# Kernel tuning notes

Measured on AMD Instinct MI355X. Metric: run time of the kernel, lower is better.

Reference implementation:

```python
import jax, jax.numpy as jnp
import numpy as np

HEADS = 16
D_H = 64
ALPHA = 1.0


def _skew(QEr):
    # Music-Transformer skew: (b,h,n,n) -> relative-to-absolute
    b, h, i, j = QEr.shape
    pad = jnp.pad(QEr, ((0, 0), (0, 0), (0, 0), (1, 0)))  # (b,h,i,j+1)
    return pad.reshape(b, h, j + 1, i)[:, :, 1:, :]  # (b,h,i,j)


def _gather_bias(q, table, idx, heads):
    # q: (b,h,i,d); table: (S,d); idx: (b,i,j) int -> (b,h,i,j)
    b, h, i, d = q.shape
    QE = jnp.einsum('bhid,sd->bhis', q, table)  # (b,h,i,S)
    idx_b = jnp.broadcast_to(idx[:, None, :, :], (b, h, i, idx.shape[-1]))
    return jnp.take_along_axis(QE, idx_b, axis=-1)


def setup_inputs() -> dict:
    key = jax.random.key(0)
    ks = jax.random.split(key, 16)
    b, n, dim = 2, 1024, 1024
    d_h = dim // HEADS
    inp = {
        'x': jax.random.normal(ks[0], (b, n, dim), dtype=jnp.float32),
        'rel_bar': jax.random.randint(ks[1], (b, n, n), 0, 17, dtype=jnp.int32),
        'rel_position': jax.random.randint(ks[2], (b, n, n), 0, 96, dtype=jnp.int32),
        'rel_octave': jax.random.randint(ks[3], (b, n, n), 0, 25, dtype=jnp.int32),
        'rel_semitone': jax.random.randint(ks[4], (b, n, n), 0, 13, dtype=jnp.int32),
        'Wq': jax.random.normal(ks[5], (dim, dim), dtype=jnp.float32) * 0.02,
        'Wk': jax.random.normal(ks[6], (dim, dim), dtype=jnp.float32) * 0.02,
        'Wv': jax.random.normal(ks[7], (dim, dim), dtype=jnp.float32) * 0.02,
        'Wo': jax.random.normal(ks[8], (dim, dim), dtype=jnp.float32) * 0.02,
        'Er': jax.random.normal(ks[9], (n, d_h), dtype=jnp.float32),
        'Er_bar': jax.random.normal(ks[10], (16, d_h), dtype=jnp.float32),
        'Er_position': jax.random.normal(ks[11], (95, d_h), dtype=jnp.float32),
        'Er_octave': jax.random.normal(ks[12], (24, d_h), dtype=jnp.float32),
        'Er_semitone': jax.random.normal(ks[13], (12, d_h), dtype=jnp.float32),
    }
    return inp


def reference(x, rel_bar, rel_position, rel_octave, rel_semitone,
              Wq, Wk, Wv, Wo, Er, Er_bar, Er_position, Er_octave, Er_semitone):
    b, n, dim = x.shape
    h, d = HEADS, dim // HEADS

    def split_heads(t):
        return t.reshape(b, n, h, d).transpose(0, 2, 1, 3)  # (b,h,n,d)

    q = split_heads(x @ Wq.T)
    k = split_heads(x @ Wk.T)
    v = split_heads(x @ Wv.T)

    QK_t = jnp.einsum('bhid,bhjd->bhij', q, k)

    # relative-index bias (Music-Transformer style)
    QEr = jnp.einsum('bhid,jd->bhij', q, Er)  # start = max_seq_len - n = 0
    Srel = _skew(QEr)

    zrow = jnp.zeros((1, d), dtype=x.dtype)
    S_bar = _gather_bias(q, jnp.concatenate([Er_bar, zrow]), rel_bar, h)
    S_position = _gather_bias(q, jnp.concatenate([Er_position, zrow]), rel_position, h)
    S_octave = _gather_bias(q, jnp.concatenate([Er_octave, zrow]), rel_octave, h)
    S_semitone = _gather_bias(q, jnp.concatenate([Er_semitone, zrow]), rel_semitone, h)

    S_time = S_bar + S_position
    S_pitch = S_octave + S_semitone

    scores = (QK_t + Srel + ALPHA * (S_time + S_pitch)) / jnp.sqrt(jnp.asarray(d, x.dtype))
    causal = jnp.tril(jnp.ones((n, n), dtype=bool))
    scores = jnp.where(causal[None, None], scores, jnp.asarray(-1e9, x.dtype))
    attn = jax.nn.softmax(scores, axis=-1)

    out = jnp.einsum('bhij,bhjd->bhid', attn, v)
    out = out.transpose(0, 2, 1, 3).reshape(b, n, dim)
    return out @ Wo.T
```

## Files before the change

kernel.cpp:

```cpp
#include <hip/hip_runtime.h>


using bf16x8 = __attribute__((ext_vector_type(8))) short;
using f32x4  = __attribute__((ext_vector_type(4))) float;

__device__ __forceinline__ float bf2f(unsigned short u) {
  unsigned x = ((unsigned)u) << 16;
  float f;
  __builtin_memcpy(&f, &x, 4);
  return f;
}
__device__ __forceinline__ unsigned short f2bf(float f) {
  unsigned x;
  __builtin_memcpy(&x, &f, 4);
  unsigned r = (x + 0x7FFFu + ((x >> 16) & 1u)) >> 16;
  return (unsigned short)r;
}

union B8 { bf16x8 v; unsigned short u[8]; };

__global__ __launch_bounds__(256) void prep(
    const float* __restrict__ x,  const float* __restrict__ Wq,
    const float* __restrict__ Wk, const float* __restrict__ Wv,
    const float* __restrict__ Wo, const float* __restrict__ Er,
    const int* __restrict__ rb, const int* __restrict__ rp,
    const int* __restrict__ ro, const int* __restrict__ rs,
    const float* __restrict__ Tb, const float* __restrict__ Tp,
    const float* __restrict__ To, const float* __restrict__ Ts,
    unsigned short* __restrict__ x_bf, unsigned short* __restrict__ Wqkv,
    unsigned short* __restrict__ Wo_bf, unsigned short* __restrict__ Er_bf,
    unsigned* __restrict__ Pidx, unsigned short* __restrict__ Tpad)
{
  const int bid = blockIdx.x;
  const int tid = threadIdx.x;
  if (bid < 1024) {
    const int total = 1589248;
    for (int i = bid * 256 + tid; i < total; i += 1024 * 256) {
      const float4* s4;
      ushort4* d4;
      if (i < 524288)       { s4 = (const float4*)x  + i;           d4 = (ushort4*)x_bf  + i; }
      else if (i < 786432)  { s4 = (const float4*)Wq + (i-524288);  d4 = (ushort4*)Wqkv  + (i-524288); }
      else if (i < 1048576) { s4 = (const float4*)Wk + (i-786432);  d4 = (ushort4*)Wqkv  + (i-786432) + 262144; }
      else if (i < 1310720) { s4 = (const float4*)Wv + (i-1048576); d4 = (ushort4*)Wqkv  + (i-1048576) + 524288; }
      else if (i < 1572864) { s4 = (const float4*)Wo + (i-1310720); d4 = (ushort4*)Wo_bf + (i-1310720); }
      else                  { s4 = (const float4*)Er + (i-1572864); d4 = (ushort4*)Er_bf + (i-1572864); }
      const float4 v = *s4;
      ushort4 o;
      o.x = f2bf(v.x); o.y = f2bf(v.y); o.z = f2bf(v.z); o.w = f2bf(v.w);
      *d4 = o;
    }
  } else if (bid < 2048) {
    for (int i = (bid - 1024) * 256 + tid; i < 524288; i += 1024 * 256) {
      const int4 a = ((const int4*)rb)[i];
      const int4 b = ((const int4*)rp)[i];
      const int4 c = ((const int4*)ro)[i];
      const int4 d = ((const int4*)rs)[i];
      uint4 r;
      r.x = (unsigned)(a.x | (17+b.x)<<5 | (113+c.x)<<12 | (138+d.x)<<20);
      r.y = (unsigned)(a.y | (17+b.y)<<5 | (113+c.y)<<12 | (138+d.y)<<20);
      r.z = (unsigned)(a.z | (17+b.z)<<5 | (113+c.z)<<12 | (138+d.z)<<20);
      r.w = (unsigned)(a.w | (17+b.w)<<5 | (113+c.w)<<12 | (138+d.w)<<20);
      ((uint4*)Pidx)[i] = r;
    }
  } else {
    for (int t = tid; t < 10240; t += 256) {
      const int s = t >> 6, d = t & 63;
      float v = 0.f;
      if (s < 16)       v = Tb[s * 64 + d];
      else if (s == 16) v = 0.f;
      else if (s < 112) v = Tp[(s - 17) * 64 + d];
      else if (s < 113) v = 0.f;
      else if (s < 137) v = To[(s - 113) * 64 + d];
      else if (s < 138) v = 0.f;
      else if (s < 150) v = Ts[(s - 138) * 64 + d];
      Tpad[t] = f2bf(v * 0.125f);
    }
  }
}

__device__ __forceinline__ void ld_lds16(const unsigned short* g, unsigned short* l) {
  __builtin_amdgcn_global_load_lds(
      (const __attribute__((address_space(1))) unsigned int*)g,
      (__attribute__((address_space(3))) unsigned int*)l, 16, 0, 0);
}

template <int MODE>
__global__ __launch_bounds__(256) void gemm128(const unsigned short* __restrict__ A,
                                               const unsigned short* __restrict__ B,
                                               void* __restrict__ Cv,
                                               int M, int N, int K)
{
  __shared__ __align__(16) unsigned short Atile[128 * 32];
  __shared__ __align__(16) unsigned short Btile[128 * 32];
  const int tid = threadIdx.x;
  const int w = tid >> 6, lane = tid & 63;
  const int c15 = lane & 15, q = lane >> 4;
  const int wr = w >> 1, wc = w & 1;
  const int n0 = blockIdx.x * 128, m0 = blockIdx.y * 128;

  const unsigned short* ag = A + (size_t)(m0 + (tid >> 2)) * K + (tid & 3) * 8;
  const unsigned short* bg = B + (size_t)(n0 + (tid >> 2)) * K + (tid & 3) * 8;
  unsigned short* al = &Atile[tid * 8];
  unsigned short* bl = &Btile[tid * 8];
  const size_t half = (size_t)64 * K;

  f32x4 acc[4][4];
  #pragma unroll
  for (int mt = 0; mt < 4; mt++)
    #pragma unroll
    for (int nt = 0; nt < 4; nt++) { acc[mt][nt][0]=0.f; acc[mt][nt][1]=0.f; acc[mt][nt][2]=0.f; acc[mt][nt][3]=0.f; }

  for (int k0 = 0; k0 < K; k0 += 32) {
    __syncthreads();
    ld_lds16(ag + k0, al);
    ld_lds16(ag + half + k0, al + 2048);
    ld_lds16(bg + k0, bl);
    ld_lds16(bg + half + k0, bl + 2048);
    __syncthreads();

    bf16x8 af[4], bfr[4];
    #pragma unroll
    for (int mt = 0; mt < 4; mt++)
      af[mt] = *(const bf16x8*)&Atile[(wr * 64 + mt * 16 + c15) * 32 + q * 8];
    #pragma unroll
    for (int nt = 0; nt < 4; nt++)
      bfr[nt] = *(const bf16x8*)&Btile[(wc * 64 + nt * 16 + c15) * 32 + q * 8];
    #pragma unroll
    for (int mt = 0; mt < 4; mt++)
      #pragma unroll
      for (int nt = 0; nt < 4; nt++)
        acc[mt][nt] = __builtin_amdgcn_mfma_f32_16x16x32_bf16(af[mt], bfr[nt], acc[mt][nt], 0, 0, 0);
  }

  #pragma unroll
  for (int mt = 0; mt < 4; mt++)
    #pragma unroll
    for (int nt = 0; nt < 4; nt++)
      #pragma unroll
      for (int r = 0; r < 4; r++) {
        const int m = m0 + wr * 64 + mt * 16 + q * 4 + r;
        const int n = n0 + wc * 64 + nt * 16 + c15;
        if constexpr (MODE == 1) {
          ((float*)Cv)[(size_t)m * N + n] = acc[mt][nt][r];
        } else {
          const int which = n >> 10, hh = (n >> 6) & 15, d = n & 63;
          const int bb = m >> 10, i = m & 1023;
          ((unsigned short*)Cv)[(size_t)which * 2097152 +
                                (((size_t)(bb << 4) + hh) << 16) + (i << 6) + d] = f2bf(acc[mt][nt][r]);
        }
      }
}

__global__ __launch_bounds__(256) void transpose_v(const unsigned short* __restrict__ V,
                                                   unsigned short* __restrict__ Vt)
{
  __shared__ unsigned short T[64][72];
  const int bh = blockIdx.x >> 4;
  const int i0 = (blockIdx.x & 15) << 6;
  const int tid = threadIdx.x;
  const int row = tid >> 2, cs = (tid & 3) * 16;
  const unsigned short* src = V + ((size_t)bh << 16) + ((size_t)(i0 + row) << 6) + cs;
  *(bf16x8*)&T[row][cs]     = *(const bf16x8*)src;
  *(bf16x8*)&T[row][cs + 8] = *(const bf16x8*)(src + 8);
  __syncthreads();
  B8 o0, o1;
  #pragma unroll
  for (int e = 0; e < 8; e++) { o0.u[e] = T[cs + e][row]; o1.u[e] = T[cs + 8 + e][row]; }
  unsigned short* dst = Vt + ((size_t)bh << 16) + ((size_t)row << 10) + i0 + cs;
  *(bf16x8*)dst       = o0.v;
  *(bf16x8*)(dst + 8) = o1.v;
}

__global__ __launch_bounds__(256) void qe_gemm(const unsigned short* __restrict__ Qh,
                                               const unsigned short* __restrict__ Tpad,
                                               unsigned short* __restrict__ QE)
{
  __shared__ __align__(16) unsigned short T[160][72];
  const int tid = threadIdx.x;
  const int w = tid >> 6, lane = tid & 63;
  const int c15 = lane & 15, q = lane >> 4;
  const int m0 = blockIdx.x * 64 + w * 16;

  for (int t = tid; t < 1280; t += 256) {
    const int r = t >> 3, c = (t & 7) * 8;
    *(bf16x8*)&T[r][c] = *(const bf16x8*)(Tpad + r * 64 + c);
  }
  __syncthreads();

  bf16x8 a0, a1;
  {
    const unsigned short* ap = Qh + ((size_t)(m0 + c15) << 6) + q * 8;
    a0 = *(const bf16x8*)ap;
    a1 = *(const bf16x8*)(ap + 32);
  }
  unsigned short* out = QE + (size_t)m0 * 160;
  #pragma unroll
  for (int st = 0; st < 10; st++) {
    bf16x8 b0 = *(const bf16x8*)&T[st * 16 + c15][q * 8];
    bf16x8 b1 = *(const bf16x8*)&T[st * 16 + c15][32 + q * 8];
    f32x4 acc; acc[0]=0.f; acc[1]=0.f; acc[2]=0.f; acc[3]=0.f;
    acc = __builtin_amdgcn_mfma_f32_16x16x32_bf16(a0, b0, acc, 0, 0, 0);
    acc = __builtin_amdgcn_mfma_f32_16x16x32_bf16(a1, b1, acc, 0, 0, 0);
    #pragma unroll
    for (int r = 0; r < 4; r++) {
      const _Float16 hv = (_Float16)acc[r];
      unsigned short hb;
      __builtin_memcpy(&hb, &hv, 2);
      out[(size_t)(q * 4 + r) * 160 + st * 16 + c15] = hb;
    }
  }
}

__global__ __launch_bounds__(256, 4) void attn_kernel(
    const unsigned short* __restrict__ QKVh,
    const unsigned short* __restrict__ Vt,
    const unsigned short* __restrict__ QE,
    const unsigned* __restrict__ Pidx,
    const unsigned short* __restrict__ Er,
    unsigned short* __restrict__ Ob)
{
  const int h  = blockIdx.x;
  const int bb = blockIdx.z;
  const int it = bb ? (15 - (int)blockIdx.y) : (int)blockIdx.y;
  const int i0 = it << 6;
  const int tid = threadIdx.x;
  const int w = tid >> 6;
  const int lane = tid & 63;
  const int c15 = lane & 15;
  const int q = lane >> 4;
  const int rowq = q * 4;

  __shared__ __align__(16) unsigned short Klds[64][72];
  __shared__ __align__(16) unsigned short C2[4][16 * 88];
  __shared__ __align__(16) unsigned short qeh[64 * 160];
  unsigned short* c2w = &C2[w][0];

  const unsigned short* qhb  = QKVh + (((size_t)(bb << 4) + h) << 16);
  const unsigned short* khb  = qhb + 2097152;
  const unsigned short* vthb = Vt + (((size_t)(bb << 4) + h) << 16);

  {
    const size_t qeoff = ((((size_t)(bb << 4) + h) * 1024) + i0) * 160;
    const unsigned short* src = QE + qeoff;
    for (int t = tid; t < 1280; t += 256)
      *(bf16x8*)&qeh[t * 8] = *(const bf16x8*)(src + t * 8);
  }

  bf16x8 qf[2];
  {
    const unsigned short* qp = qhb + ((size_t)(i0 + w * 16 + c15) << 6);
    #pragma unroll
    for (int kk = 0; kk < 2; kk++) {
      B8 t;
      t.v = *(const bf16x8*)(qp + kk * 32 + q * 8);
      #pragma unroll
      for (int e = 0; e < 8; e++) t.u[e] = f2bf(bf2f(t.u[e]) * 0.125f);
      qf[kk] = t.v;
    }
  }

  f32x4 Oa[4];
  float mrow[4], lrow[4];
  #pragma unroll
  for (int dt = 0; dt < 4; dt++) { Oa[dt][0]=0.f; Oa[dt][1]=0.f; Oa[dt][2]=0.f; Oa[dt][3]=0.f; }
  #pragma unroll
  for (int r = 0; r < 4; r++) { mrow[r] = -3e38f; lrow[r] = 0.f; }

  const int iw = i0 + w * 16;
  const size_t idx0 = ((size_t)bb << 20) + ((size_t)(iw + rowq) << 10);

  for (int jt = 0; jt <= it; jt++) {
    const int j0 = jt << 6;

    unsigned pv[4][4];
    #pragma unroll
    for (int nt = 0; nt < 4; nt++)
      #pragma unroll
      for (int r = 0; r < 4; r++)
        pv[nt][r] = Pidx[idx0 + ((size_t)r << 10) + j0 + nt * 16 + c15];
    bf16x8 vf[4][2];
    #pragma unroll
    for (int dt = 0; dt < 4; dt++) {
      const unsigned short* vp = vthb + ((size_t)(dt * 16 + c15) << 10) + j0 + q * 8;
      vf[dt][0] = *(const bf16x8*)vp;
      vf[dt][1] = *(const bf16x8*)(vp + 32);
    }

    __syncthreads();

    {
      const unsigned short* kt = khb + (j0 << 6);
      *(bf16x8*)&Klds[tid >> 3][(tid & 7) * 8]        = *(const bf16x8*)(kt + tid * 8);
      *(bf16x8*)&Klds[32 + (tid >> 3)][(tid & 7) * 8] = *(const bf16x8*)(kt + 2048 + tid * 8);
    }
    __syncthreads();

    f32x4 S[4];
    #pragma unroll
    for (int nt = 0; nt < 4; nt++) {
      f32x4 a; a[0]=0.f; a[1]=0.f; a[2]=0.f; a[3]=0.f;
      bf16x8 k0 = *(const bf16x8*)&Klds[nt * 16 + c15][q * 8];
      bf16x8 k1 = *(const bf16x8*)&Klds[nt * 16 + c15][32 + q * 8];
      a = __builtin_amdgcn_mfma_f32_16x16x32_bf16(qf[0], k0, a, 0, 0, 0);
      a = __builtin_amdgcn_mfma_f32_16x16x32_bf16(qf[1], k1, a, 0, 0, 0);
      S[nt] = a;
    }

    {
      const int rbase = 960 - i0 + j0;
      #pragma unroll
      for (int t5 = 0; t5 < 5; t5++) {
        const int pt = 3 - w + t5;
        int row = rbase + pt * 16 + c15;
        row = row > 1023 ? 1023 : row;
        const unsigned short* ep = Er + (row << 6) + q * 8;
        bf16x8 e0 = *(const bf16x8*)ep;
        bf16x8 e1 = *(const bf16x8*)(ep + 32);
        f32x4 a; a[0]=0.f; a[1]=0.f; a[2]=0.f; a[3]=0.f;
        a = __builtin_amdgcn_mfma_f32_16x16x32_bf16(qf[0], e0, a, 0, 0, 0);
        a = __builtin_amdgcn_mfma_f32_16x16x32_bf16(qf[1], e1, a, 0, 0, 0);
        #pragma unroll
        for (int r = 0; r < 4; r++)
          c2w[(rowq + r) * 88 + t5 * 16 + c15] = f2bf(a[r]);
      }
    }

    #pragma unroll
    for (int nt = 0; nt < 4; nt++) {
      const int j = j0 + nt * 16 + c15;
      #pragma unroll
      for (int r = 0; r < 4; r++) {
        const int rb = (w * 16 + rowq + r) * 160;
        const unsigned p = pv[nt][r];
        _Float16 q0, q1, q2, q3;
        __builtin_memcpy(&q0, &qeh[rb + (p & 31)], 2);
        __builtin_memcpy(&q1, &qeh[rb + ((p >> 5) & 127)], 2);
        __builtin_memcpy(&q2, &qeh[rb + ((p >> 12) & 255)], 2);
        __builtin_memcpy(&q3, &qeh[rb + (p >> 20)], 2);
        const float bias = (float)(q0 + q1) + (float)(q2 + q3);
        const float srel = bf2f(c2w[(rowq + r) * 88 + (15 - (rowq + r) + nt * 16 + c15)]);
        float sc = S[nt][r] + srel + bias;
        if (jt == it && j > iw + rowq + r) sc = -3e38f;
        S[nt][r] = sc;
      }
    }

    float alpha[4];
    #pragma unroll
    for (int r = 0; r < 4; r++) {
      float v = fmaxf(fmaxf(S[0][r], S[1][r]), fmaxf(S[2][r], S[3][r]));
      v = fmaxf(v, __shfl_xor(v, 1));
      v = fmaxf(v, __shfl_xor(v, 2));
      v = fmaxf(v, __shfl_xor(v, 4));
      v = fmaxf(v, __shfl_xor(v, 8));
      const float mn = fmaxf(mrow[r], v);
      alpha[r] = __expf(mrow[r] - mn);
      mrow[r] = mn;
    }
    #pragma unroll
    for (int nt = 0; nt < 4; nt++)
      #pragma unroll
      for (int r = 0; r < 4; r++)
        S[nt][r] = __expf(S[nt][r] - mrow[r]);
    #pragma unroll
    for (int r = 0; r < 4; r++) {
      float s = S[0][r] + S[1][r] + S[2][r] + S[3][r];
      s += __shfl_xor(s, 1);
      s += __shfl_xor(s, 2);
      s += __shfl_xor(s, 4);
      s += __shfl_xor(s, 8);
      lrow[r] = lrow[r] * alpha[r] + s;
      #pragma unroll
      for (int dt = 0; dt < 4; dt++) Oa[dt][r] *= alpha[r];
    }

    #pragma unroll
    for (int nt = 0; nt < 4; nt++)
      #pragma unroll
      for (int r = 0; r < 4; r++)
        c2w[(rowq + r) * 88 + nt * 16 + c15] = f2bf(S[nt][r]);

    bf16x8 pf[2];
    #pragma unroll
    for (int kk = 0; kk < 2; kk++)
      pf[kk] = *(const bf16x8*)&c2w[c15 * 88 + kk * 32 + q * 8];

    #pragma unroll
    for (int dt = 0; dt < 4; dt++) {
      Oa[dt] = __builtin_amdgcn_mfma_f32_16x16x32_bf16(pf[0], vf[dt][0], Oa[dt], 0, 0, 0);
      Oa[dt] = __builtin_amdgcn_mfma_f32_16x16x32_bf16(pf[1], vf[dt][1], Oa[dt], 0, 0, 0);
    }
  }

  #pragma unroll
  for (int dt = 0; dt < 4; dt++)
    #pragma unroll
    for (int r = 0; r < 4; r++) {
      const int i_ = iw + rowq + r;
      const float o = Oa[dt][r] / lrow[r];
      Ob[(((size_t)bb << 10) + i_) * 1024 + (h << 6) + dt * 16 + c15] = f2bf(o);
    }
}

extern "C" void kernel_launch(void* const* d_in, const int* in_sizes, int n_in,
                              void* d_out, int out_size, void* d_ws, size_t ws_size,
                              hipStream_t stream)
{
  const float* x    = (const float*)d_in[0];
  const int*   rbar = (const int*)d_in[1];
  const int*   rpos = (const int*)d_in[2];
  const int*   roct = (const int*)d_in[3];
  const int*   rsem = (const int*)d_in[4];
  const float* Wq   = (const float*)d_in[5];
  const float* Wk   = (const float*)d_in[6];
  const float* Wv   = (const float*)d_in[7];
  const float* Wo   = (const float*)d_in[8];
  const float* Er   = (const float*)d_in[9];
  const float* Tb   = (const float*)d_in[10];
  const float* Tp   = (const float*)d_in[11];
  const float* To   = (const float*)d_in[12];
  const float* Ts   = (const float*)d_in[13];
  float* out = (float*)d_out;

  char* ws = (char*)d_ws;
  const size_t MB = 1u << 20;
  unsigned short* x_bf    = (unsigned short*)(ws);
  unsigned short* Vt      = (unsigned short*)(ws);
  unsigned short* Wqkv_bf = (unsigned short*)(ws + 4 * MB);
  unsigned short* Wo_bf   = (unsigned short*)(ws + 10 * MB);
  unsigned short* Er_bf   = (unsigned short*)(ws + 12 * MB);
  unsigned short* Tpad    = (unsigned short*)(ws + 12 * MB + 256 * 1024);
  unsigned short* QKVh    = (unsigned short*)(ws + 13 * MB);
  unsigned short* Ob      = (unsigned short*)(ws + 25 * MB);
  unsigned short* QE      = (unsigned short*)(ws + 29 * MB);
  unsigned*       Pidx    = (unsigned*)(ws + 39 * MB);

  prep<<<2049, 256, 0, stream>>>(x, Wq, Wk, Wv, Wo, Er, rbar, rpos, roct, rsem,
                                 Tb, Tp, To, Ts,
                                 x_bf, Wqkv_bf, Wo_bf, Er_bf, Pidx, Tpad);

  gemm128<2><<<dim3(24, 16), 256, 0, stream>>>(x_bf, Wqkv_bf, QKVh, 2048, 3072, 1024);
  transpose_v<<<512, 256, 0, stream>>>(QKVh + 2 * 2097152, Vt);
  qe_gemm<<<512, 256, 0, stream>>>(QKVh, Tpad, QE);
  attn_kernel<<<dim3(16, 16, 2), 256, 0, stream>>>(QKVh, Vt, QE, Pidx, Er_bf, Ob);
  gemm128<1><<<dim3(8, 16), 256, 0, stream>>>(Ob, Wo_bf, out, 2048, 1024, 1024);
}
```

Before: 301.0 us.

## Narrow GEMM N-tile to 64 and drop K LDS staging in attention

Adds a BN template parameter to the GEMM and launches both projection GEMMs with 128x64 tiles, doubling the block count to fill more CUs on the small problem. In the attention kernel, K tiles are now read straight from global memory instead of being staged through LDS with two barriers per step. The Pidx and V loads move next to their use to cut register pressure, and the occupancy hint of 4 in launch_bounds is removed. The costs are less latency hiding, since loads are no longer issued early, and more redundant K reads from global/L2 across the four waves.

```diff
diff --git a/kernel.cpp b/kernel.cpp
--- a/kernel.cpp
+++ b/kernel.cpp
@@ -84,19 +84,20 @@
       (__attribute__((address_space(3))) unsigned int*)l, 16, 0, 0);
 }
 
-template <int MODE>
+template <int MODE, int BN>
 __global__ __launch_bounds__(256) void gemm128(const unsigned short* __restrict__ A,
                                                const unsigned short* __restrict__ B,
                                                void* __restrict__ Cv,
                                                int M, int N, int K)
 {
+  constexpr int NT = BN / 32;
   __shared__ __align__(16) unsigned short Atile[128 * 32];
-  __shared__ __align__(16) unsigned short Btile[128 * 32];
+  __shared__ __align__(16) unsigned short Btile[BN * 32];
   const int tid = threadIdx.x;
   const int w = tid >> 6, lane = tid & 63;
   const int c15 = lane & 15, q = lane >> 4;
   const int wr = w >> 1, wc = w & 1;
-  const int n0 = blockIdx.x * 128, m0 = blockIdx.y * 128;
+  const int n0 = blockIdx.x * BN, m0 = blockIdx.y * 128;
 
   const unsigned short* ag = A + (size_t)(m0 + (tid >> 2)) * K + (tid & 3) * 8;
   const unsigned short* bg = B + (size_t)(n0 + (tid >> 2)) * K + (tid & 3) * 8;
@@ -104,42 +105,42 @@
   unsigned short* bl = &Btile[tid * 8];
   const size_t half = (size_t)64 * K;
 
-  f32x4 acc[4][4];
+  f32x4 acc[4][NT];
   #pragma unroll
   for (int mt = 0; mt < 4; mt++)
     #pragma unroll
-    for (int nt = 0; nt < 4; nt++) { acc[mt][nt][0]=0.f; acc[mt][nt][1]=0.f; acc[mt][nt][2]=0.f; acc[mt][nt][3]=0.f; }
+    for (int nt = 0; nt < NT; nt++) { acc[mt][nt][0]=0.f; acc[mt][nt][1]=0.f; acc[mt][nt][2]=0.f; acc[mt][nt][3]=0.f; }
 
   for (int k0 = 0; k0 < K; k0 += 32) {
     __syncthreads();
     ld_lds16(ag + k0, al);
     ld_lds16(ag + half + k0, al + 2048);
     ld_lds16(bg + k0, bl);
-    ld_lds16(bg + half + k0, bl + 2048);
+    if constexpr (BN == 128) ld_lds16(bg + half + k0, bl + 2048);
     __syncthreads();
 
-    bf16x8 af[4], bfr[4];
+    bf16x8 af[4], bfr[NT];
     #pragma unroll
     for (int mt = 0; mt < 4; mt++)
       af[mt] = *(const bf16x8*)&Atile[(wr * 64 + mt * 16 + c15) * 32 + q * 8];
     #pragma unroll
-    for (int nt = 0; nt < 4; nt++)
-      bfr[nt] = *(const bf16x8*)&Btile[(wc * 64 + nt * 16 + c15) * 32 + q * 8];
+    for (int nt = 0; nt < NT; nt++)
+      bfr[nt] = *(const bf16x8*)&Btile[(wc * (BN / 2) + nt * 16 + c15) * 32 + q * 8];
     #pragma unroll
     for (int mt = 0; mt < 4; mt++)
       #pragma unroll
-      for (int nt = 0; nt < 4; nt++)
+      for (int nt = 0; nt < NT; nt++)
         acc[mt][nt] = __builtin_amdgcn_mfma_f32_16x16x32_bf16(af[mt], bfr[nt], acc[mt][nt], 0, 0, 0);
   }
 
   #pragma unroll
   for (int mt = 0; mt < 4; mt++)
     #pragma unroll
-    for (int nt = 0; nt < 4; nt++)
+    for (int nt = 0; nt < NT; nt++)
       #pragma unroll
       for (int r = 0; r < 4; r++) {
         const int m = m0 + wr * 64 + mt * 16 + q * 4 + r;
-        const int n = n0 + wc * 64 + nt * 16 + c15;
+        const int n = n0 + wc * (BN / 2) + nt * 16 + c15;
         if constexpr (MODE == 1) {
           ((float*)Cv)[(size_t)m * N + n] = acc[mt][nt][r];
         } else {
@@ -211,7 +212,7 @@
   }
 }
 
-__global__ __launch_bounds__(256, 4) void attn_kernel(
+__global__ __launch_bounds__(256) void attn_kernel(
     const unsigned short* __restrict__ QKVh,
     const unsigned short* __restrict__ Vt,
     const unsigned short* __restrict__ QE,
@@ -230,7 +231,6 @@
   const int q = lane >> 4;
   const int rowq = q * 4;
 
-  __shared__ __align__(16) unsigned short Klds[64][72];
   __shared__ __align__(16) unsigned short C2[4][16 * 88];
   __shared__ __align__(16) unsigned short qeh[64 * 160];
   unsigned short* c2w = &C2[w][0];
@@ -269,38 +269,18 @@
   const int iw = i0 + w * 16;
   const size_t idx0 = ((size_t)bb << 20) + ((size_t)(iw + rowq) << 10);
 
+  __syncthreads();
+
   for (int jt = 0; jt <= it; jt++) {
     const int j0 = jt << 6;
 
-    unsigned pv[4][4];
-    #pragma unroll
-    for (int nt = 0; nt < 4; nt++)
-      #pragma unroll
-      for (int r = 0; r < 4; r++)
-        pv[nt][r] = Pidx[idx0 + ((size_t)r << 10) + j0 + nt * 16 + c15];
-    bf16x8 vf[4][2];
-    #pragma unroll
-    for (int dt = 0; dt < 4; dt++) {
-      const unsigned short* vp = vthb + ((size_t)(dt * 16 + c15) << 10) + j0 + q * 8;
-      vf[dt][0] = *(const bf16x8*)vp;
-      vf[dt][1] = *(const bf16x8*)(vp + 32);
-    }
-
-    __syncthreads();
-
-    {
-      const unsigned short* kt = khb + (j0 << 6);
-      *(bf16x8*)&Klds[tid >> 3][(tid & 7) * 8]        = *(const bf16x8*)(kt + tid * 8);
-      *(bf16x8*)&Klds[32 + (tid >> 3)][(tid & 7) * 8] = *(const bf16x8*)(kt + 2048 + tid * 8);
-    }
-    __syncthreads();
-
     f32x4 S[4];
     #pragma unroll
     for (int nt = 0; nt < 4; nt++) {
+      const unsigned short* kp = khb + ((size_t)(j0 + nt * 16 + c15) << 6) + q * 8;
+      bf16x8 k0 = *(const bf16x8*)kp;
+      bf16x8 k1 = *(const bf16x8*)(kp + 32);
       f32x4 a; a[0]=0.f; a[1]=0.f; a[2]=0.f; a[3]=0.f;
-      bf16x8 k0 = *(const bf16x8*)&Klds[nt * 16 + c15][q * 8];
-      bf16x8 k1 = *(const bf16x8*)&Klds[nt * 16 + c15][32 + q * 8];
       a = __builtin_amdgcn_mfma_f32_16x16x32_bf16(qf[0], k0, a, 0, 0, 0);
       a = __builtin_amdgcn_mfma_f32_16x16x32_bf16(qf[1], k1, a, 0, 0, 0);
       S[nt] = a;
@@ -328,10 +308,14 @@
     #pragma unroll
     for (int nt = 0; nt < 4; nt++) {
       const int j = j0 + nt * 16 + c15;
+      unsigned pv[4];
+      #pragma unroll
+      for (int r = 0; r < 4; r++)
+        pv[r] = Pidx[idx0 + ((size_t)r << 10) + j];
       #pragma unroll
       for (int r = 0; r < 4; r++) {
         const int rb = (w * 16 + rowq + r) * 160;
-        const unsigned p = pv[nt][r];
+        const unsigned p = pv[r];
         _Float16 q0, q1, q2, q3;
         __builtin_memcpy(&q0, &qeh[rb + (p & 31)], 2);
         __builtin_memcpy(&q1, &qeh[rb + ((p >> 5) & 127)], 2);
@@ -387,8 +371,11 @@
 
     #pragma unroll
     for (int dt = 0; dt < 4; dt++) {
-      Oa[dt] = __builtin_amdgcn_mfma_f32_16x16x32_bf16(pf[0], vf[dt][0], Oa[dt], 0, 0, 0);
-      Oa[dt] = __builtin_amdgcn_mfma_f32_16x16x32_bf16(pf[1], vf[dt][1], Oa[dt], 0, 0, 0);
+      const unsigned short* vp = vthb + ((size_t)(dt * 16 + c15) << 10) + j0 + q * 8;
+      bf16x8 v0 = *(const bf16x8*)vp;
+      bf16x8 v1 = *(const bf16x8*)(vp + 32);
+      Oa[dt] = __builtin_amdgcn_mfma_f32_16x16x32_bf16(pf[0], v0, Oa[dt], 0, 0, 0);
+      Oa[dt] = __builtin_amdgcn_mfma_f32_16x16x32_bf16(pf[1], v1, Oa[dt], 0, 0, 0);
     }
   }
 
@@ -439,9 +426,9 @@
                                  Tb, Tp, To, Ts,
                                  x_bf, Wqkv_bf, Wo_bf, Er_bf, Pidx, Tpad);
 
-  gemm128<2><<<dim3(24, 16), 256, 0, stream>>>(x_bf, Wqkv_bf, QKVh, 2048, 3072, 1024);
+  gemm128<2, 64><<<dim3(48, 16), 256, 0, stream>>>(x_bf, Wqkv_bf, QKVh, 2048, 3072, 1024);
   transpose_v<<<512, 256, 0, stream>>>(QKVh + 2 * 2097152, Vt);
   qe_gemm<<<512, 256, 0, stream>>>(QKVh, Tpad, QE);
   attn_kernel<<<dim3(16, 16, 2), 256, 0, stream>>>(QKVh, Vt, QE, Pidx, Er_bf, Ob);
-  gemm128<1><<<dim3(8, 16), 256, 0, stream>>>(Ob, Wo_bf, out, 2048, 1024, 1024);
-}
+  gemm128<1, 64><<<dim3(16, 16), 256, 0, stream>>>(Ob, Wo_bf, out, 2048, 1024, 1024);
+}
```

Measured after the change: 291.3 us. 3.2% less time.
